# Performance work log

Measured on AMD Instinct MI355X. Metric: run time of the kernel, lower is better.

## Reference

```python
import jax, jax.numpy as jnp
import numpy as np


def setup_inputs() -> dict:
    key = jax.random.key(0)
    k1, k2 = jax.random.split(key)
    B, HW, C, M, P = 8, 4096, 1024, 32, 512
    feature_map = jax.random.normal(k1, (B, HW, C), dtype=jnp.float32)
    # normalized (y, x) coords in [0,1], as produced by mask.nonzero()/[H,W]
    point_coords = jax.random.uniform(k2, (B, M, P, 2), dtype=jnp.float32)
    return {"feature_map": feature_map, "point_coords": point_coords}


def reference(feature_map, point_coords):
    # feature_map: [B, H*W, C]; point_coords: [B, M, P, 2] as (y_norm, x_norm).
    B, HW, C = feature_map.shape
    h = w = int(np.sqrt(HW))
    # torch flips coords to (x, y); grid_sample(align_corners=True) maps
    # grid g = 2*coord-1 to pixel coord*(size-1).
    y = point_coords[..., 0] * (h - 1)  # [B, M, P]
    x = point_coords[..., 1] * (w - 1)
    x0f = jnp.floor(x)
    y0f = jnp.floor(y)
    wx = (x - x0f)[..., None]  # [B, M, P, 1]
    wy = (y - y0f)[..., None]
    ix0 = jnp.clip(x0f.astype(jnp.int32), 0, w - 1)
    ix1 = jnp.clip(ix0 + 1, 0, w - 1)
    iy0 = jnp.clip(y0f.astype(jnp.int32), 0, h - 1)
    iy1 = jnp.clip(iy0 + 1, 0, h - 1)

    def gather(iy, ix):
        idx = (iy * w + ix).reshape(B, -1)  # [B, M*P]
        g = jnp.take_along_axis(feature_map, idx[:, :, None], axis=1)  # [B, M*P, C]
        return g.reshape(B, iy.shape[1], iy.shape[2], C)

    f00 = gather(iy0, ix0)
    f01 = gather(iy0, ix1)
    f10 = gather(iy1, ix0)
    f11 = gather(iy1, ix1)
    # bilinear interpolation -> [B, M, P, C]
    sampled = (f00 * (1 - wx) * (1 - wy) + f01 * wx * (1 - wy)
               + f10 * (1 - wx) * wy + f11 * wx * wy)
    # AdaptiveAvgPool1d(1) over points, then transpose -> [B, M, 1, C]
    region_feat = jnp.mean(sampled, axis=2, keepdims=True)
    return region_feat
```

## Files before the change

### kernel.cpp

```cpp
#include <hip/hip_runtime.h>


#define NB 8
#define NM 32
#define NP 512
#define NC 1024
#define NH 64
#define NHW 4096

#define KC   256
#define NKC  (NHW / KC)
#define CT   256
#define NCT  (NC / CT)
#define PF   8

__global__ __launch_bounds__(256) void scatter_w(
    const float* __restrict__ pc, float* __restrict__ W)
{
    int idx = blockIdx.x * 256 + threadIdx.x;
    int bm  = idx >> 9;
    int m   = bm & (NM - 1);
    int b   = bm >> 5;

    float2 c = ((const float2*)pc)[idx];
    float y = c.x * 63.0f;
    float x = c.y * 63.0f;
    float x0f = floorf(x), y0f = floorf(y);
    float wx = x - x0f, wy = y - y0f;
    int ix0 = min(max((int)x0f, 0), 63);
    int ix1 = min(ix0 + 1, 63);
    int iy0 = min(max((int)y0f, 0), 63);
    int iy1 = min(iy0 + 1, 63);
    float wx1 = 1.0f - wx, wy1 = 1.0f - wy;
    const float s = 1.0f / (float)NP;

    float* Wb = W + (size_t)b * (NHW * NM) + m;
    atomicAdd(Wb + ((iy0 * NH + ix0) * NM), wx1 * wy1 * s);
    atomicAdd(Wb + ((iy0 * NH + ix1) * NM), wx  * wy1 * s);
    atomicAdd(Wb + ((iy1 * NH + ix0) * NM), wx1 * wy  * s);
    atomicAdd(Wb + ((iy1 * NH + ix1) * NM), wx  * wy  * s);
}

__global__ __launch_bounds__(256, 2) void wgemm(
    const float* __restrict__ W, const float* __restrict__ F,
    float* __restrict__ P)
{
    __shared__ float4 sW[KC * NM / 4];

    const int kc  = blockIdx.x;
    const int ct  = blockIdx.y;
    const int b   = blockIdx.z;
    const int tid = threadIdx.x;
    const int c   = ct * CT + tid;
    const int hw0 = kc * KC;

    const float4* Wg = (const float4*)(W + ((size_t)b * NHW + hw0) * NM);
#pragma unroll
    for (int j = 0; j < 8; ++j)
        sW[tid + 256 * j] = Wg[tid + 256 * j];
    __syncthreads();

    const float* Fb = F + ((size_t)b * NHW + hw0) * NC + c;

    float acc[NM];
#pragma unroll
    for (int m = 0; m < NM; ++m) acc[m] = 0.0f;

    float fbuf[PF];
#pragma unroll
    for (int j = 0; j < PF; ++j) fbuf[j] = Fb[(size_t)j * NC];

    for (int i = 0; i < KC; i += PF) {
        float fcur[PF];
#pragma unroll
        for (int j = 0; j < PF; ++j) fcur[j] = fbuf[j];
        if (i + PF < KC) {
#pragma unroll
            for (int j = 0; j < PF; ++j)
                fbuf[j] = Fb[(size_t)(i + PF + j) * NC];
        }
#pragma unroll
        for (int j = 0; j < PF; ++j) {
            const float4* w4 = sW + (i + j) * (NM / 4);
            float f = fcur[j];
#pragma unroll
            for (int mq = 0; mq < NM / 4; ++mq) {
                float4 w = w4[mq];
                acc[mq * 4 + 0] = fmaf(w.x, f, acc[mq * 4 + 0]);
                acc[mq * 4 + 1] = fmaf(w.y, f, acc[mq * 4 + 1]);
                acc[mq * 4 + 2] = fmaf(w.z, f, acc[mq * 4 + 2]);
                acc[mq * 4 + 3] = fmaf(w.w, f, acc[mq * 4 + 3]);
            }
        }
    }

    float* pb = P + (((size_t)kc * NB + b) * NM) * NC + c;
#pragma unroll
    for (int m = 0; m < NM; ++m)
        pb[(size_t)m * NC] = acc[m];
}

__global__ __launch_bounds__(256) void reduce_p(
    const float* __restrict__ P, float* __restrict__ out)
{
    const int idx = blockIdx.x * 256 + threadIdx.x;
    const float4* p4 = (const float4*)P;
    const int stride = NB * NM * NC / 4;
    float4 s = make_float4(0.f, 0.f, 0.f, 0.f);
#pragma unroll
    for (int kc = 0; kc < NKC; ++kc) {
        float4 v = p4[(size_t)kc * stride + idx];
        s.x += v.x; s.y += v.y; s.z += v.z; s.w += v.w;
    }
    ((float4*)out)[idx] = s;
}

__global__ __launch_bounds__(256) void region_pool_direct(
    const float* __restrict__ fm, const float* __restrict__ pc,
    float* __restrict__ out)
{
    __shared__ int4   sIdx[NP];
    __shared__ float4 sWt[NP];
    const int bid = blockIdx.x;
    const int b   = bid >> 5;
    const int tid = threadIdx.x;
    const float2* pc2 = (const float2*)(pc + (size_t)bid * NP * 2);
    for (int p = tid; p < NP; p += 256) {
        float2 c = pc2[p];
        float y = c.x * 63.0f, x = c.y * 63.0f;
        float x0f = floorf(x), y0f = floorf(y);
        float wx = x - x0f, wy = y - y0f;
        int ix0 = min(max((int)x0f, 0), 63);
        int ix1 = min(ix0 + 1, 63);
        int iy0 = min(max((int)y0f, 0), 63);
        int iy1 = min(iy0 + 1, 63);
        sIdx[p] = make_int4((iy0 * NH + ix0) << 10, (iy0 * NH + ix1) << 10,
                            (iy1 * NH + ix0) << 10, (iy1 * NH + ix1) << 10);
        float wx1 = 1.0f - wx, wy1 = 1.0f - wy;
        sWt[p] = make_float4(wx1 * wy1, wx * wy1, wx1 * wy, wx * wy);
    }
    __syncthreads();
    const float* Fb = fm + (size_t)b * (NHW * NC) + tid * 4;
    float4 acc = make_float4(0.f, 0.f, 0.f, 0.f);
#pragma unroll 4
    for (int p = 0; p < NP; ++p) {
        int4 off = sIdx[p]; float4 w = sWt[p];
        float4 f00 = *(const float4*)(Fb + off.x);
        float4 f01 = *(const float4*)(Fb + off.y);
        float4 f10 = *(const float4*)(Fb + off.z);
        float4 f11 = *(const float4*)(Fb + off.w);
        acc.x = fmaf(w.x, f00.x, fmaf(w.y, f01.x, fmaf(w.z, f10.x, fmaf(w.w, f11.x, acc.x))));
        acc.y = fmaf(w.x, f00.y, fmaf(w.y, f01.y, fmaf(w.z, f10.y, fmaf(w.w, f11.y, acc.y))));
        acc.z = fmaf(w.x, f00.z, fmaf(w.y, f01.z, fmaf(w.z, f10.z, fmaf(w.w, f11.z, acc.z))));
        acc.w = fmaf(w.x, f00.w, fmaf(w.y, f01.w, fmaf(w.z, f10.w, fmaf(w.w, f11.w, acc.w))));
    }
    const float inv = 1.0f / (float)NP;
    ((float4*)(out + (size_t)bid * NC))[tid] =
        make_float4(acc.x * inv, acc.y * inv, acc.z * inv, acc.w * inv);
}

extern "C" void kernel_launch(void* const* d_in, const int* in_sizes, int n_in,
                              void* d_out, int out_size, void* d_ws, size_t ws_size,
                              hipStream_t stream) {
    const float* fm = (const float*)d_in[0];
    const float* pc = (const float*)d_in[1];
    float* out = (float*)d_out;

    const size_t wbytes = (size_t)NB * NHW * NM * sizeof(float);
    const size_t pbytes = (size_t)NKC * NB * NM * NC * sizeof(float);
    if (ws_size >= wbytes + pbytes) {
        float* W = (float*)d_ws;
        float* P = (float*)((char*)d_ws + wbytes);
        hipMemsetAsync(W, 0, wbytes, stream);
        scatter_w<<<(NB * NM * NP) / 256, 256, 0, stream>>>(pc, W);
        dim3 grid(NKC, NCT, NB);
        wgemm<<<grid, CT, 0, stream>>>(W, fm, P);
        reduce_p<<<(NB * NM * NC / 4) / 256, 256, 0, stream>>>(P, out);
    } else {
        region_pool_direct<<<NB * NM, 256, 0, stream>>>(fm, pc, out);
    }
}
```

Baseline: 232.5 us.

## Compute two channels per thread in wgemm and read weights directly from global

Each wgemm thread now accumulates two adjacent channels with float2 feature loads, which doubles register accumulators and halves the number of column tiles. The shared-memory staging of the weight tile is dropped in favour of uniform global float4 reads, which may become scalar loads. KC is halved, so there are twice as many K-chunk partials and reduce_p sums more of them. The aim is more FMA work per weight load and less LDS traffic, at the cost of higher register pressure, possibly lower occupancy, and a larger partial buffer.

```diff
diff --git a/kernel.cpp b/kernel.cpp
--- a/kernel.cpp
+++ b/kernel.cpp
@@ -8,11 +8,13 @@
 #define NH 64
 #define NHW 4096
 
-#define KC   256
-#define NKC  (NHW / KC)
-#define CT   256
-#define NCT  (NC / CT)
-#define PF   8
+#define KC    128
+#define NKC   (NHW / KC)
+#define CPT   2
+#define CT    256
+#define CTILE (CT * CPT)
+#define NCT   (NC / CTILE)
+#define PF    8
 
 __global__ __launch_bounds__(256) void scatter_w(
     const float* __restrict__ pc, float* __restrict__ W)
@@ -45,51 +47,52 @@
     const float* __restrict__ W, const float* __restrict__ F,
     float* __restrict__ P)
 {
-    __shared__ float4 sW[KC * NM / 4];
-
     const int kc  = blockIdx.x;
     const int ct  = blockIdx.y;
     const int b   = blockIdx.z;
     const int tid = threadIdx.x;
-    const int c   = ct * CT + tid;
+    const int c   = ct * CTILE + tid * CPT;
     const int hw0 = kc * KC;
 
-    const float4* Wg = (const float4*)(W + ((size_t)b * NHW + hw0) * NM);
+    const float4* __restrict__ Wk =
+        (const float4*)(W + ((size_t)b * NHW + hw0) * NM);
+
+    const float2* __restrict__ Fb =
+        (const float2*)(F + ((size_t)b * NHW + hw0) * NC + c);
+    const int fstride = NC / 2;
+
+    float accx[NM], accy[NM];
 #pragma unroll
-    for (int j = 0; j < 8; ++j)
-        sW[tid + 256 * j] = Wg[tid + 256 * j];
-    __syncthreads();
+    for (int m = 0; m < NM; ++m) { accx[m] = 0.0f; accy[m] = 0.0f; }
 
-    const float* Fb = F + ((size_t)b * NHW + hw0) * NC + c;
-
-    float acc[NM];
+    float2 fbuf[PF];
 #pragma unroll
-    for (int m = 0; m < NM; ++m) acc[m] = 0.0f;
-
-    float fbuf[PF];
-#pragma unroll
-    for (int j = 0; j < PF; ++j) fbuf[j] = Fb[(size_t)j * NC];
+    for (int j = 0; j < PF; ++j) fbuf[j] = Fb[(size_t)j * fstride];
 
     for (int i = 0; i < KC; i += PF) {
-        float fcur[PF];
+        float2 fcur[PF];
 #pragma unroll
         for (int j = 0; j < PF; ++j) fcur[j] = fbuf[j];
         if (i + PF < KC) {
 #pragma unroll
             for (int j = 0; j < PF; ++j)
-                fbuf[j] = Fb[(size_t)(i + PF + j) * NC];
+                fbuf[j] = Fb[(size_t)(i + PF + j) * fstride];
         }
 #pragma unroll
         for (int j = 0; j < PF; ++j) {
-            const float4* w4 = sW + (i + j) * (NM / 4);
-            float f = fcur[j];
+            const float4* __restrict__ w4 = Wk + (i + j) * (NM / 4);
+            float2 f = fcur[j];
 #pragma unroll
-            for (int mq = 0; mq < NM / 4; ++mq) {
-                float4 w = w4[mq];
-                acc[mq * 4 + 0] = fmaf(w.x, f, acc[mq * 4 + 0]);
-                acc[mq * 4 + 1] = fmaf(w.y, f, acc[mq * 4 + 1]);
-                acc[mq * 4 + 2] = fmaf(w.z, f, acc[mq * 4 + 2]);
-                acc[mq * 4 + 3] = fmaf(w.w, f, acc[mq * 4 + 3]);
+            for (int q = 0; q < NM / 4; ++q) {
+                float4 w = w4[q];
+                accx[q * 4 + 0] = fmaf(w.x, f.x, accx[q * 4 + 0]);
+                accy[q * 4 + 0] = fmaf(w.x, f.y, accy[q * 4 + 0]);
+                accx[q * 4 + 1] = fmaf(w.y, f.x, accx[q * 4 + 1]);
+                accy[q * 4 + 1] = fmaf(w.y, f.y, accy[q * 4 + 1]);
+                accx[q * 4 + 2] = fmaf(w.z, f.x, accx[q * 4 + 2]);
+                accy[q * 4 + 2] = fmaf(w.z, f.y, accy[q * 4 + 2]);
+                accx[q * 4 + 3] = fmaf(w.w, f.x, accx[q * 4 + 3]);
+                accy[q * 4 + 3] = fmaf(w.w, f.y, accy[q * 4 + 3]);
             }
         }
     }
@@ -97,7 +100,7 @@
     float* pb = P + (((size_t)kc * NB + b) * NM) * NC + c;
 #pragma unroll
     for (int m = 0; m < NM; ++m)
-        pb[(size_t)m * NC] = acc[m];
+        *(float2*)(pb + (size_t)m * NC) = make_float2(accx[m], accy[m]);
 }
 
 __global__ __launch_bounds__(256) void reduce_p(
```

After: 242.5 us. 1.04x slower.

## Retile weighted GEMM to 8 channels by 8 regions per thread

Applied to the files above, without the earlier changes.

The GEMM kernel moves from one channel and all 32 regions per thread to 8 channels (two float4 loads) and 8 regions per thread. The four region groups in a block share one channel tile. The K chunk is halved to 128, so there are twice as many partial sums for reduce_p to add, and the channel tile grows to 512. The intent is vectorized 16-byte feature loads and fewer shared-memory weight reads per FMA. In exchange, each feature row is now loaded by four thread groups instead of one, which raises global or cache traffic, and the partial-sum buffer doubles.

```diff
diff --git a/kernel.cpp b/kernel.cpp
--- a/kernel.cpp
+++ b/kernel.cpp
@@ -8,11 +8,13 @@
 #define NH 64
 #define NHW 4096
 
-#define KC   256
-#define NKC  (NHW / KC)
-#define CT   256
-#define NCT  (NC / CT)
-#define PF   8
+#define KC    128
+#define NKC   (NHW / KC)
+#define CPT   8
+#define MT    8
+#define CTILE 512
+#define NCT   (NC / CTILE)
+#define PF    4
 
 __global__ __launch_bounds__(256) void scatter_w(
     const float* __restrict__ pc, float* __restrict__ W)
@@ -45,59 +47,83 @@
     const float* __restrict__ W, const float* __restrict__ F,
     float* __restrict__ P)
 {
-    __shared__ float4 sW[KC * NM / 4];
-
-    const int kc  = blockIdx.x;
-    const int ct  = blockIdx.y;
-    const int b   = blockIdx.z;
-    const int tid = threadIdx.x;
-    const int c   = ct * CT + tid;
-    const int hw0 = kc * KC;
-
-    const float4* Wg = (const float4*)(W + ((size_t)b * NHW + hw0) * NM);
-#pragma unroll
-    for (int j = 0; j < 8; ++j)
-        sW[tid + 256 * j] = Wg[tid + 256 * j];
+    __shared__ float sW[KC * NM];
+
+    const int kc   = blockIdx.x;
+    const int ct   = blockIdx.y;
+    const int b    = blockIdx.z;
+    const int tid  = threadIdx.x;
+    const int mq   = tid >> 6;
+    const int lane = tid & 63;
+    const int c0   = ct * CTILE + lane * CPT;
+    const int hw0  = kc * KC;
+
+    {
+        const float4* Wg = (const float4*)(W + ((size_t)b * NHW + hw0) * NM);
+        float4* sW4 = (float4*)sW;
+#pragma unroll
+        for (int j = 0; j < 4; ++j)
+            sW4[tid + 256 * j] = Wg[tid + 256 * j];
+    }
     __syncthreads();
 
-    const float* Fb = F + ((size_t)b * NHW + hw0) * NC + c;
-
-    float acc[NM];
-#pragma unroll
-    for (int m = 0; m < NM; ++m) acc[m] = 0.0f;
-
-    float fbuf[PF];
-#pragma unroll
-    for (int j = 0; j < PF; ++j) fbuf[j] = Fb[(size_t)j * NC];
+    const float4* __restrict__ Fb =
+        (const float4*)(F + ((size_t)b * NHW + hw0) * NC + c0);
+    const int fstride = NC / 4;
+
+    float4 acc[MT][2];
+#pragma unroll
+    for (int m = 0; m < MT; ++m) {
+        acc[m][0] = make_float4(0.f, 0.f, 0.f, 0.f);
+        acc[m][1] = make_float4(0.f, 0.f, 0.f, 0.f);
+    }
+
+    float4 fbuf[PF][2];
+#pragma unroll
+    for (int j = 0; j < PF; ++j) {
+        fbuf[j][0] = Fb[(size_t)j * fstride];
+        fbuf[j][1] = Fb[(size_t)j * fstride + 1];
+    }
+
+    const float4* sWq = (const float4*)(sW + mq * MT);
 
     for (int i = 0; i < KC; i += PF) {
-        float fcur[PF];
-#pragma unroll
-        for (int j = 0; j < PF; ++j) fcur[j] = fbuf[j];
-        if (i + PF < KC) {
-#pragma unroll
-            for (int j = 0; j < PF; ++j)
-                fbuf[j] = Fb[(size_t)(i + PF + j) * NC];
-        }
 #pragma unroll
         for (int j = 0; j < PF; ++j) {
-            const float4* w4 = sW + (i + j) * (NM / 4);
-            float f = fcur[j];
-#pragma unroll
-            for (int mq = 0; mq < NM / 4; ++mq) {
-                float4 w = w4[mq];
-                acc[mq * 4 + 0] = fmaf(w.x, f, acc[mq * 4 + 0]);
-                acc[mq * 4 + 1] = fmaf(w.y, f, acc[mq * 4 + 1]);
-                acc[mq * 4 + 2] = fmaf(w.z, f, acc[mq * 4 + 2]);
-                acc[mq * 4 + 3] = fmaf(w.w, f, acc[mq * 4 + 3]);
+            const int s = i + j;
+            float4 wa0 = sWq[(size_t)s * (NM / 4)];
+            float4 wa1 = sWq[(size_t)s * (NM / 4) + 1];
+
+            float4 f0 = fbuf[j][0];
+            float4 f1 = fbuf[j][1];
+            if (i + PF < KC) {
+                fbuf[j][0] = Fb[(size_t)(s + PF) * fstride];
+                fbuf[j][1] = Fb[(size_t)(s + PF) * fstride + 1];
+            }
+
+            const float wm[MT] = { wa0.x, wa0.y, wa0.z, wa0.w,
+                                   wa1.x, wa1.y, wa1.z, wa1.w };
+#pragma unroll
+            for (int m = 0; m < MT; ++m) {
+                float w = wm[m];
+                acc[m][0].x = fmaf(w, f0.x, acc[m][0].x);
+                acc[m][0].y = fmaf(w, f0.y, acc[m][0].y);
+                acc[m][0].z = fmaf(w, f0.z, acc[m][0].z);
+                acc[m][0].w = fmaf(w, f0.w, acc[m][0].w);
+                acc[m][1].x = fmaf(w, f1.x, acc[m][1].x);
+                acc[m][1].y = fmaf(w, f1.y, acc[m][1].y);
+                acc[m][1].z = fmaf(w, f1.z, acc[m][1].z);
+                acc[m][1].w = fmaf(w, f1.w, acc[m][1].w);
             }
         }
     }
 
-    float* pb = P + (((size_t)kc * NB + b) * NM) * NC + c;
-#pragma unroll
-    for (int m = 0; m < NM; ++m)
-        pb[(size_t)m * NC] = acc[m];
+    float* pb = P + (((size_t)kc * NB + b) * NM + mq * MT) * NC + c0;
+#pragma unroll
+    for (int mm = 0; mm < MT; ++mm) {
+        ((float4*)(pb + (size_t)mm * NC))[0] = acc[mm][0];
+        ((float4*)(pb + (size_t)mm * NC))[1] = acc[mm][1];
+    }
 }
 
 __global__ __launch_bounds__(256) void reduce_p(
@@ -174,7 +200,7 @@
         hipMemsetAsync(W, 0, wbytes, stream);
         scatter_w<<<(NB * NM * NP) / 256, 256, 0, stream>>>(pc, W);
         dim3 grid(NKC, NCT, NB);
-        wgemm<<<grid, CT, 0, stream>>>(W, fm, P);
+        wgemm<<<grid, 256, 0, stream>>>(W, fm, P);
         reduce_p<<<(NB * NM * NC / 4) / 256, 256, 0, stream>>>(P, out);
     } else {
         region_pool_direct<<<NB * NM, 256, 0, stream>>>(fm, pc, out);
```

After: 250.3 us. 7.7% more time.
